# Kernel optimization log

Measured on AMD Instinct MI355X. Metric: run time of the kernel, lower is better.

The kernel has to match this reference:

```python
import jax, jax.numpy as jnp
import numpy as np

HIDDEN = 128
B, N, S = 4, 200, 512  # batch, 200 segments, 512 tokens each (hard-coded in source view())


def setup_inputs() -> dict:
    key = jax.random.key(0)
    ks = jax.random.split(key, 7)
    query = jax.random.normal(ks[0], (B, HIDDEN), dtype=jnp.float32)
    context = jax.random.normal(ks[1], (B, N, S, HIDDEN), dtype=jnp.float32)
    context_mask = jax.random.uniform(ks[2], (B, N, S), dtype=jnp.float32)
    scale = 1.0 / np.sqrt(HIDDEN)
    Wq = jax.random.normal(ks[3], (HIDDEN, HIDDEN), dtype=jnp.float32) * scale
    bq = jax.random.normal(ks[4], (HIDDEN,), dtype=jnp.float32) * 0.01
    Wc = jax.random.normal(ks[5], (HIDDEN, HIDDEN), dtype=jnp.float32) * scale
    bc = jax.random.normal(ks[6], (HIDDEN,), dtype=jnp.float32) * 0.01
    return {"query": query, "context": context, "context_mask": context_mask,
            "Wq": Wq, "bq": bq, "Wc": Wc, "bc": bc}


def reference(query, context, context_mask, Wq, bq, Wc, bc):
    # q_projection / c_projection (nn.Linear: x @ W.T + b)
    q = query @ Wq.T + bq                      # [B, H]
    c = context @ Wc.T + bc                    # [B, N, S, H]
    # bmm(reshape_c, q) -> scores [B, N, S]
    att = jnp.einsum('bnsh,bh->bns', c, q)
    masked_att = att * context_mask            # multiplicative mask (as in source)
    w = jax.nn.softmax(masked_att, axis=-1)    # [B, N, S]
    # fused dual-axis weighted reductions (avoid [B,N,S,H] broadcast materialization)
    result = jnp.einsum('bns,bnsh->bnh', w, context)       # sum over tokens S
    token_result = jnp.einsum('bns,bnsh->bsh', w, context)  # sum over segments N
    return (result, token_result)
```

## Files before the change

kernel.cpp:

```cpp
#include <hip/hip_runtime.h>
#include <hip/hip_bf16.h>
#include <math.h>

#define H    128
#define NB   4
#define NSEG 200
#define NS   512
#define GN   10
#define GS   32
#define NGRP (NSEG / GN)
#define NST  (NS / GS)


__global__ __launch_bounds__(512)
void scores_softmax_kernel(const float* __restrict__ context,
                           const float* __restrict__ mask,
                           const float* __restrict__ query,
                           const float* __restrict__ Wq,
                           const float* __restrict__ bq,
                           const float* __restrict__ Wc,
                           const float* __restrict__ bc,
                           float* __restrict__ w_out) {
    __shared__ float  qsh[H];
    __shared__ float4 vv4[32];
    __shared__ float  mk[NS];
    __shared__ float  sc[NS];
    __shared__ float  wred[8];
    __shared__ float  c0sh;

    const int tid = threadIdx.x;
    const int blk = blockIdx.x;
    const int b   = blk / NSEG;
    const float* cseg = context + (size_t)blk * NS * H;

    if (tid < H) {
        float acc = bq[tid];
        const float* qr = query + b * H;
        const float* wr = Wq + tid * H;
        #pragma unroll 4
        for (int k = 0; k < H; ++k) acc += qr[k] * wr[k];
        qsh[tid] = acc;
    }
    mk[tid] = mask[(size_t)blk * NS + tid];
    __syncthreads();
    if (tid < H) {
        float vacc = 0.f;
        #pragma unroll 4
        for (int h2 = 0; h2 < H; ++h2) vacc += qsh[h2] * Wc[h2 * H + tid];
        ((float*)vv4)[tid] = vacc;
    }
    if (tid < 64) {
        float p = qsh[tid] * bc[tid] + qsh[tid + 64] * bc[tid + 64];
        for (int o = 32; o > 0; o >>= 1) p += __shfl_xor(p, o);
        if (tid == 0) c0sh = p;
    }
    __syncthreads();

    const int   h4  = tid & 31;
    const int   rg  = tid >> 5;
    const float c0b = c0sh;

    #pragma unroll 4
    for (int it = 0; it < NS / 16; ++it) {
        const int s = it * 16 + rg;
        const float4 cv = ((const float4*)(cseg + (size_t)s * H))[h4];
        const float4 vq = vv4[h4];
        float p = cv.x * vq.x + cv.y * vq.y + cv.z * vq.z + cv.w * vq.w;
        p += __shfl_xor(p, 16);
        p += __shfl_xor(p, 8);
        p += __shfl_xor(p, 4);
        p += __shfl_xor(p, 2);
        p += __shfl_xor(p, 1);
        if (h4 == 0) sc[s] = (p + c0b) * mk[s];
    }
    __syncthreads();

    const float x = sc[tid];
    float m = x;
    for (int o = 32; o > 0; o >>= 1) m = fmaxf(m, __shfl_xor(m, o));
    const int wid = tid >> 6, lane = tid & 63;
    if (lane == 0) wred[wid] = m;
    __syncthreads();
    if (tid == 0) {
        float mm = wred[0];
        for (int i = 1; i < 8; ++i) mm = fmaxf(mm, wred[i]);
        wred[0] = mm;
    }
    __syncthreads();
    const float mx = wred[0];
    const float e  = __expf(x - mx);
    float ssum = e;
    for (int o = 32; o > 0; o >>= 1) ssum += __shfl_xor(ssum, o);
    __syncthreads();
    if (lane == 0) wred[wid] = ssum;
    __syncthreads();
    if (tid == 0) {
        float t = 0.f;
        for (int i = 0; i < 8; ++i) t += wred[i];
        wred[0] = t;
    }
    __syncthreads();
    w_out[(size_t)blk * NS + tid] = e / wred[0];
}

__global__ __launch_bounds__(256)
void weighted_kernel(const float* __restrict__ context,
                     const float* __restrict__ w,
                     float* __restrict__ result_part,
                     float* __restrict__ token_part) {
    const int bid = blockIdx.x;
    const int st  = bid & (NST - 1);
    const int tmp = bid / NST;
    const int ng  = tmp % NGRP;
    const int b   = tmp / NGRP;
    const int n0  = ng * GN;
    const int s0  = st * GS;

    const int tid = threadIdx.x;
    const int h4  = tid & 31;
    const int rg  = tid >> 5;

    __shared__ float  wt[GN * GS];
    __shared__ float4 red4[5 * 8 * 32];

    for (int i = tid; i < GN * GS; i += 256) {
        const int nn = i >> 5, ss = i & (GS - 1);
        wt[i] = w[((size_t)(b * NSEG + n0 + nn)) * NS + s0 + ss];
    }
    __syncthreads();

    float4 racc[GN];
    float4 tacc[4];
    #pragma unroll
    for (int n = 0; n < GN; ++n) racc[n] = make_float4(0.f, 0.f, 0.f, 0.f);
    #pragma unroll
    for (int j = 0; j < 4; ++j) tacc[j] = make_float4(0.f, 0.f, 0.f, 0.f);

    #pragma unroll
    for (int n = 0; n < GN; ++n) {
        const float* base = context + ((size_t)(b * NSEG + n0 + n) * NS + s0) * (size_t)H;
        #pragma unroll
        for (int j = 0; j < 4; ++j) {
            const int s = j * 8 + rg;
            const float  wv = wt[n * GS + s];
            const float4 cv = ((const float4*)(base + (size_t)s * H))[h4];
            racc[n].x += wv * cv.x; racc[n].y += wv * cv.y;
            racc[n].z += wv * cv.z; racc[n].w += wv * cv.w;
            tacc[j].x += wv * cv.x; tacc[j].y += wv * cv.y;
            tacc[j].z += wv * cv.z; tacc[j].w += wv * cv.w;
        }
    }

    #pragma unroll
    for (int j = 0; j < 4; ++j) {
        const int s = j * 8 + rg;
        ((float4*)token_part)[(((size_t)ng * NB + b) * NS + s0 + s) * 32 + h4] = tacc[j];
    }

    for (int nb = 0; nb < GN; nb += 5) {
        #pragma unroll
        for (int j = 0; j < 5; ++j)
            red4[(j * 8 + rg) * 32 + h4] = racc[nb + j];
        __syncthreads();
        for (int off = 4; off > 0; off >>= 1) {
            if (rg < off) {
                #pragma unroll
                for (int j = 0; j < 5; ++j) {
                    float4 o = red4[(j * 8 + rg + off) * 32 + h4];
                    float4 mm = red4[(j * 8 + rg) * 32 + h4];
                    mm.x += o.x; mm.y += o.y; mm.z += o.z; mm.w += o.w;
                    red4[(j * 8 + rg) * 32 + h4] = mm;
                }
            }
            __syncthreads();
        }
        if (rg == 0) {
            #pragma unroll
            for (int j = 0; j < 5; ++j)
                ((float4*)result_part)[(((size_t)(b * NSEG + n0 + nb + j)) * NST + st) * 32 + h4]
                    = red4[(j * 8) * 32 + h4];
        }
        __syncthreads();
    }
}

__global__ __launch_bounds__(256)
void combine_kernel(const float* __restrict__ rpart,
                    const float* __restrict__ tpart,
                    float* __restrict__ out) {
    const int RQ = NB * NSEG * H / 4;
    const int i  = blockIdx.x * 256 + threadIdx.x;
    if (i < RQ) {
        const int row = i >> 5, h4 = i & 31;
        float4 acc = {0.f, 0.f, 0.f, 0.f};
        const float4* p = (const float4*)rpart;
        #pragma unroll
        for (int st = 0; st < NST; ++st) {
            float4 o = p[((size_t)row * NST + st) * 32 + h4];
            acc.x += o.x; acc.y += o.y; acc.z += o.z; acc.w += o.w;
        }
        ((float4*)out)[i] = acc;
    } else {
        const int j = i - RQ;
        float4 acc = {0.f, 0.f, 0.f, 0.f};
        const float4* p = (const float4*)tpart;
        #pragma unroll
        for (int g = 0; g < NGRP; ++g) {
            float4 o = p[(size_t)g * (NB * NS * H / 4) + j];
            acc.x += o.x; acc.y += o.y; acc.z += o.z; acc.w += o.w;
        }
        ((float4*)out)[i] = acc;
    }
}

extern "C" void kernel_launch(void* const* d_in, const int* in_sizes, int n_in,
                              void* d_out, int out_size, void* d_ws, size_t ws_size,
                              hipStream_t stream) {
    const float* query   = (const float*)d_in[0];
    const float* context = (const float*)d_in[1];
    const float* mask    = (const float*)d_in[2];
    const float* Wq      = (const float*)d_in[3];
    const float* bq      = (const float*)d_in[4];
    const float* Wc      = (const float*)d_in[5];
    const float* bc      = (const float*)d_in[6];

    float* out = (float*)d_out;
    float* wsf = (float*)d_ws;

    float* w     = wsf;
    float* rpart = wsf + NB * NSEG * NS;
    float* tpart = rpart + NB * NSEG * NST * H;

    scores_softmax_kernel<<<NB * NSEG, 512, 0, stream>>>(
        context, mask, query, Wq, bq, Wc, bc, w);
    weighted_kernel<<<NB * NGRP * NST, 256, 0, stream>>>(context, w, rpart, tpart);
    const int total4 = NB * NSEG * H / 4 + NB * NS * H / 4;
    combine_kernel<<<total4 / 256, 256, 0, stream>>>(rpart, tpart, out);
}
```

Measured before the change: 359.3 us.

## Hoist query projection into a precompute kernel and double segment grouping

Moves the per-batch query projection and Wc folding out of each of the 800 scores blocks into a small precompute kernel that writes v and c0 to workspace, so each block only loads 128 floats instead of doing two 128x128 matvecs. It also doubles GN from 10 to 20, which halves the number of token partials and the combine work for the token-axis reduction, at the cost of fewer weighted-kernel blocks and more registers per thread. The combine grid size now rounds up. An extra kernel launch is added.

```diff
diff --git a/kernel.cpp b/kernel.cpp
--- a/kernel.cpp
+++ b/kernel.cpp
@@ -6,65 +6,69 @@
 #define NB   4
 #define NSEG 200
 #define NS   512
-#define GN   10
+#define GN   20
 #define GS   32
 #define NGRP (NSEG / GN)
 #define NST  (NS / GS)
 
 
+__global__ void precompute_kernel(const float* __restrict__ query,
+                                  const float* __restrict__ Wq,
+                                  const float* __restrict__ bq,
+                                  const float* __restrict__ Wc,
+                                  const float* __restrict__ bc,
+                                  float* __restrict__ v_out,
+                                  float* __restrict__ c0_out) {
+    __shared__ float qsh[H];
+    const int tid = threadIdx.x;
+    const int b   = blockIdx.x;
+    float acc = bq[tid];
+    const float* qr = query + b * H;
+    const float* wr = Wq + tid * H;
+    #pragma unroll 4
+    for (int k = 0; k < H; ++k) acc += qr[k] * wr[k];
+    qsh[tid] = acc;
+    __syncthreads();
+    float vacc = 0.f;
+    #pragma unroll 4
+    for (int h2 = 0; h2 < H; ++h2) vacc += qsh[h2] * Wc[h2 * H + tid];
+    v_out[b * H + tid] = vacc;
+    if (tid < 64) {
+        float p = qsh[tid] * bc[tid] + qsh[tid + 64] * bc[tid + 64];
+        for (int o = 32; o > 0; o >>= 1) p += __shfl_xor(p, o);
+        if (tid == 0) c0_out[b] = p;
+    }
+}
+
 __global__ __launch_bounds__(512)
 void scores_softmax_kernel(const float* __restrict__ context,
                            const float* __restrict__ mask,
-                           const float* __restrict__ query,
-                           const float* __restrict__ Wq,
-                           const float* __restrict__ bq,
-                           const float* __restrict__ Wc,
-                           const float* __restrict__ bc,
+                           const float* __restrict__ v,
+                           const float* __restrict__ c0,
                            float* __restrict__ w_out) {
-    __shared__ float  qsh[H];
     __shared__ float4 vv4[32];
     __shared__ float  mk[NS];
     __shared__ float  sc[NS];
     __shared__ float  wred[8];
-    __shared__ float  c0sh;
 
     const int tid = threadIdx.x;
     const int blk = blockIdx.x;
     const int b   = blk / NSEG;
     const float* cseg = context + (size_t)blk * NS * H;
 
-    if (tid < H) {
-        float acc = bq[tid];
-        const float* qr = query + b * H;
-        const float* wr = Wq + tid * H;
-        #pragma unroll 4
-        for (int k = 0; k < H; ++k) acc += qr[k] * wr[k];
-        qsh[tid] = acc;
-    }
+    if (tid < 32) vv4[tid] = ((const float4*)(v + b * H))[tid];
     mk[tid] = mask[(size_t)blk * NS + tid];
-    __syncthreads();
-    if (tid < H) {
-        float vacc = 0.f;
-        #pragma unroll 4
-        for (int h2 = 0; h2 < H; ++h2) vacc += qsh[h2] * Wc[h2 * H + tid];
-        ((float*)vv4)[tid] = vacc;
-    }
-    if (tid < 64) {
-        float p = qsh[tid] * bc[tid] + qsh[tid + 64] * bc[tid + 64];
-        for (int o = 32; o > 0; o >>= 1) p += __shfl_xor(p, o);
-        if (tid == 0) c0sh = p;
-    }
     __syncthreads();
 
     const int   h4  = tid & 31;
     const int   rg  = tid >> 5;
-    const float c0b = c0sh;
+    const float c0b = c0[b];
+    const float4 vq = vv4[h4];
 
     #pragma unroll 4
     for (int it = 0; it < NS / 16; ++it) {
         const int s = it * 16 + rg;
         const float4 cv = ((const float4*)(cseg + (size_t)s * H))[h4];
-        const float4 vq = vv4[h4];
         float p = cv.x * vq.x + cv.y * vq.y + cv.z * vq.z + cv.w * vq.w;
         p += __shfl_xor(p, 16);
         p += __shfl_xor(p, 8);
@@ -227,13 +231,15 @@
     float* out = (float*)d_out;
     float* wsf = (float*)d_ws;
 
-    float* w     = wsf;
-    float* rpart = wsf + NB * NSEG * NS;
+    float* v     = wsf;
+    float* c0    = wsf + 512;
+    float* w     = wsf + 1024;
+    float* rpart = w + NB * NSEG * NS;
     float* tpart = rpart + NB * NSEG * NST * H;
 
-    scores_softmax_kernel<<<NB * NSEG, 512, 0, stream>>>(
-        context, mask, query, Wq, bq, Wc, bc, w);
+    precompute_kernel<<<NB, 128, 0, stream>>>(query, Wq, bq, Wc, bc, v, c0);
+    scores_softmax_kernel<<<NB * NSEG, 512, 0, stream>>>(context, mask, v, c0, w);
     weighted_kernel<<<NB * NGRP * NST, 256, 0, stream>>>(context, w, rpart, tpart);
     const int total4 = NB * NSEG * H / 4 + NB * NS * H / 4;
-    combine_kernel<<<total4 / 256, 256, 0, stream>>>(rpart, tpart, out);
-}
+    combine_kernel<<<(total4 + 255) / 256, 256, 0, stream>>>(rpart, tpart, out);
+}
```

New measurement: 370.9 us. 3.2% more time.
